# Kernel tuning notes

Hardware: AMD Instinct MI355X
Metric: run time of the kernel (lower is better)

The kernel has to match this reference:

```python
import jax, jax.numpy as jnp
import numpy as np

N = 100_000   # nodes
E = 1_600_000 # edges per edge type
DIN = 128     # input_dim
DH = 128      # prot_hidden_dim
L = 3         # prot_num_layers
EPS = 1e-5


def setup_inputs() -> dict:
    key = jax.random.key(0)
    ks = jax.random.split(key, 8)
    s = 1.0 / np.sqrt(DH)
    return {
        "x": jax.random.normal(ks[0], (N, DIN), jnp.float32),
        "src": jax.random.randint(ks[1], (3, E), 0, N, jnp.int32),
        "dst": jax.random.randint(ks[2], (3, E), 0, N, jnp.int32),
        "gc_W0": jax.random.normal(ks[3], (3, DIN, DH), jnp.float32) * s,
        "gc_b0": jnp.zeros((3, DH), jnp.float32),
        "gc_W": jax.random.normal(ks[4], (L - 1, 3, DH, DH), jnp.float32) * s,
        "gc_b": jnp.zeros((L - 1, 3, DH), jnp.float32),
        "fc_W": jax.random.normal(ks[5], (L, DH, DH), jnp.float32) * s,
        "fc_b": jnp.zeros((L, DH), jnp.float32),
        "bn_gamma": jnp.ones((L, DH), jnp.float32),
        "bn_beta": jnp.zeros((L, DH), jnp.float32),
    }


def _graph_conv(x, src, dst, W, b):
    # DGL GraphConv, norm='both': D_in^{-1/2} A D_out^{-1/2} X W + b
    ones = jnp.ones(src.shape[0], x.dtype)
    deg_out = jnp.clip(jax.ops.segment_sum(ones, src, num_segments=N), 1.0)
    deg_in = jnp.clip(jax.ops.segment_sum(ones, dst, num_segments=N), 1.0)
    # apply weight first (same math; keeps gathered message width = DH)
    h = (x * jax.lax.rsqrt(deg_out)[:, None]) @ W  # [N, DH]
    agg = jax.ops.segment_sum(h[src], dst, num_segments=N)  # gather + scatter-add
    return agg * jax.lax.rsqrt(deg_in)[:, None] + b


def _batchnorm(x, gamma, beta):
    # training-mode BatchNorm1d: biased batch statistics
    mu = jnp.mean(x, axis=0)
    var = jnp.mean(jnp.square(x - mu), axis=0)
    return (x - mu) * jax.lax.rsqrt(var + EPS) * gamma + beta


def reference(x, src, dst, gc_W0, gc_b0, gc_W, gc_b, fc_W, fc_b, bn_gamma, bn_beta):
    h = x
    for l in range(L):
        W = gc_W0 if l == 0 else gc_W[l - 1]
        b = gc_b0 if l == 0 else gc_b[l - 1]
        # HeteroGraphConv with aggregate='sum' over 3 edge types
        out = _graph_conv(h, src[0], dst[0], W[0], b[0])
        for e in range(1, 3):
            out = out + _graph_conv(h, src[e], dst[e], W[e], b[e])
        # FC -> ReLU -> BatchNorm (dropout = identity in eval mode)
        h = _batchnorm(jax.nn.relu(out @ fc_W[l] + fc_b[l]), bn_gamma[l], bn_beta[l])
    return h
```

## Files before the change

kernel.cpp:

```cpp
#include <hip/hip_runtime.h>


#define EPSV 1e-5f
#define CH 4096
#define MAXNB 512

typedef __attribute__((ext_vector_type(8))) short s8v;
typedef __attribute__((ext_vector_type(4))) float f4v;

__global__ void coarse_hist(const int* __restrict__ src, const int* __restrict__ dst,
                            int* __restrict__ chd, int* __restrict__ chs,
                            int E, int NB) {
    __shared__ int hd[MAXNB], hs[MAXNB];
    int t = blockIdx.y;
    for (int i = threadIdx.x; i < MAXNB; i += 256) { hd[i] = 0; hs[i] = 0; }
    __syncthreads();
    int base = blockIdx.x * CH;
    int end = base + CH < E ? base + CH : E;
    const int* sp = src + (size_t)t * E;
    const int* dp = dst + (size_t)t * E;
    for (int i = base + threadIdx.x; i < end; i += 256) {
        atomicAdd(&hd[dp[i] >> 8], 1);
        atomicAdd(&hs[sp[i] >> 8], 1);
    }
    __syncthreads();
    for (int b = threadIdx.x; b < NB; b += 256) {
        if (hd[b]) atomicAdd(&chd[t * NB + b], hd[b]);
        if (hs[b]) atomicAdd(&chs[t * NB + b], hs[b]);
    }
}

__global__ void scan_off(const int* __restrict__ chd, const int* __restrict__ chs,
                         int* __restrict__ offd, int* __restrict__ offs,
                         int* __restrict__ gcd, int* __restrict__ gcs,
                         int* __restrict__ rowptr, int NB, int N, int E) {
    __shared__ int s[MAXNB];
    int tid = threadIdx.x;
    for (int a = 0; a < 6; ++a) {
        const int* h = (a < 3) ? chd + a * NB : chs + (a - 3) * NB;
        int* off = (a < 3) ? offd + a * (NB + 1) : offs + (a - 3) * (NB + 1);
        int* gc = (a < 3) ? gcd + a * NB : gcs + (a - 3) * NB;
        s[tid] = (tid < NB) ? h[tid] : 0;
        __syncthreads();
        for (int o = 1; o < MAXNB; o <<= 1) {
            int v = (tid >= o) ? s[tid - o] : 0;
            __syncthreads();
            s[tid] += v;
            __syncthreads();
        }
        if (tid < NB) {
            off[tid + 1] = s[tid];
            if (tid == 0) off[0] = 0;
        }
        __syncthreads();
        if (tid < NB) gc[tid] = off[tid];
        __syncthreads();
    }
    if (tid < 3) rowptr[tid * (N + 1) + N] = E;
}

__launch_bounds__(256)
__global__ void scatter_coarse(const int* __restrict__ src, const int* __restrict__ dst,
                               int* __restrict__ gcd, int* __restrict__ gcs,
                               int* __restrict__ dbuf, unsigned char* __restrict__ sbuf,
                               int E, int NB) {
    __shared__ int hd[MAXNB], hs[MAXNB];
    __shared__ int lod[MAXNB], los[MAXNB];
    __shared__ int bd[MAXNB], bs[MAXNB];
    __shared__ int rbi[CH];
    __shared__ unsigned char rbs[CH];
    const int tid = threadIdx.x;
    const int t = blockIdx.y;
    const int base = blockIdx.x * CH;
    const int end = base + CH < E ? base + CH : E;
    const int cnt = end - base;
    const int* sp = src + (size_t)t * E;
    const int* dp = dst + (size_t)t * E;

    for (int i = tid; i < MAXNB; i += 256) { hd[i] = 0; hs[i] = 0; }
    __syncthreads();
    for (int i = base + tid; i < end; i += 256) {
        atomicAdd(&hd[dp[i] >> 8], 1);
        atomicAdd(&hs[sp[i] >> 8], 1);
    }
    __syncthreads();
    for (int b = tid; b < NB; b += 256) {
        bd[b] = hd[b] ? atomicAdd(&gcd[t * NB + b], hd[b]) : 0;
        bs[b] = hs[b] ? atomicAdd(&gcs[t * NB + b], hs[b]) : 0;
    }
    lod[tid] = hd[tid]; lod[tid + 256] = hd[tid + 256];
    los[tid] = hs[tid]; los[tid + 256] = hs[tid + 256];
    __syncthreads();
    for (int o = 1; o < MAXNB; o <<= 1) {
        int a0 = lod[tid], a1 = lod[tid + 256];
        int b0 = los[tid], b1 = los[tid + 256];
        int p0 = (tid >= o) ? lod[tid - o] : 0;
        int p1 = lod[tid + 256 - o];
        int q0 = (tid >= o) ? los[tid - o] : 0;
        int q1 = los[tid + 256 - o];
        __syncthreads();
        lod[tid] = a0 + p0; lod[tid + 256] = a1 + p1;
        los[tid] = b0 + q0; los[tid + 256] = b1 + q1;
        __syncthreads();
    }
    hd[tid] = lod[tid] - hd[tid]; hd[tid + 256] = lod[tid + 256] - hd[tid + 256];
    hs[tid] = los[tid] - hs[tid]; hs[tid + 256] = los[tid + 256] - hs[tid + 256];
    __syncthreads();
    for (int i = base + tid; i < end; i += 256) {
        int sv = sp[i], dv = dp[i];
        int lp = atomicAdd(&hd[dv >> 8], 1);
        rbi[lp] = (sv << 8) | (dv & 255);
        int ls = atomicAdd(&hs[sv >> 8], 1);
        rbs[ls] = (unsigned char)(sv & 255);
    }
    __syncthreads();
    for (int i = tid; i < cnt; i += 256) {
        int lo = 0, hi = NB - 1;
        while (lo < hi) { int mid = (lo + hi) >> 1; if (lod[mid] > i) hi = mid; else lo = mid + 1; }
        int excl = lo ? lod[lo - 1] : 0;
        dbuf[(size_t)t * E + bd[lo] + (i - excl)] = rbi[i];
    }
    for (int i = tid; i < cnt; i += 256) {
        int lo = 0, hi = NB - 1;
        while (lo < hi) { int mid = (lo + hi) >> 1; if (los[mid] > i) hi = mid; else lo = mid + 1; }
        int excl = lo ? los[lo - 1] : 0;
        sbuf[(size_t)t * E + bs[lo] + (i - excl)] = rbs[i];
    }
}

#define FDCAP 6656
__global__ void fine_dst(const int* __restrict__ dbuf, const int* __restrict__ offd,
                         int* __restrict__ esrc, int* __restrict__ rowptr,
                         float* __restrict__ dri, int E, int N, int NB) {
    __shared__ int h[256], sc[256], cur[256];
    __shared__ int rb[FDCAP];
    int b = blockIdx.x, t = blockIdx.y;
    int tid = threadIdx.x;
    h[tid] = 0;
    __syncthreads();
    int beg = offd[t * (NB + 1) + b], end = offd[t * (NB + 1) + b + 1];
    int cnt = end - beg;
    const int* dp = dbuf + (size_t)t * E;
    for (int i = beg + tid; i < end; i += 256) atomicAdd(&h[dp[i] & 255], 1);
    __syncthreads();
    sc[tid] = h[tid];
    __syncthreads();
    for (int o = 1; o < 256; o <<= 1) {
        int v = (tid >= o) ? sc[tid - o] : 0;
        __syncthreads();
        sc[tid] += v;
        __syncthreads();
    }
    int excl = sc[tid] - h[tid];
    cur[tid] = excl;
    int node = b * 256 + tid;
    if (node < N) {
        rowptr[t * (N + 1) + node] = beg + excl;
        int dg = h[tid] < 1 ? 1 : h[tid];
        dri[(size_t)t * N + node] = rsqrtf((float)dg);
    }
    __syncthreads();
    if (cnt <= FDCAP) {
        for (int i = beg + tid; i < end; i += 256) {
            int v = dp[i];
            int p = atomicAdd(&cur[v & 255], 1);
            rb[p] = v >> 8;
        }
        __syncthreads();
        for (int i = tid; i < cnt; i += 256) esrc[(size_t)t * E + beg + i] = rb[i];
    } else {
        for (int i = beg + tid; i < end; i += 256) {
            int v = dp[i];
            int p = beg + atomicAdd(&cur[v & 255], 1);
            esrc[(size_t)t * E + p] = v >> 8;
        }
    }
}

__global__ void fine_src(const unsigned char* __restrict__ sbuf, const int* __restrict__ offs,
                         float* __restrict__ dro, int E, int N, int NB) {
    __shared__ int h[256];
    int b = blockIdx.x, t = blockIdx.y;
    int tid = threadIdx.x;
    h[tid] = 0;
    __syncthreads();
    int beg = offs[t * (NB + 1) + b], end = offs[t * (NB + 1) + b + 1];
    const unsigned char* sp = sbuf + (size_t)t * E;
    for (int i = beg + tid; i < end; i += 256) atomicAdd(&h[sp[i]], 1);
    __syncthreads();
    int node = b * 256 + tid;
    if (node < N) {
        int dg = h[tid] < 1 ? 1 : h[tid];
        dro[(size_t)t * N + node] = rsqrtf((float)dg);
    }
}

__device__ __forceinline__ unsigned int bfr(float f) {
    unsigned int u = __float_as_uint(f);
    return (u + 0x7FFFu + ((u >> 16) & 1u)) >> 16;
}
__device__ __forceinline__ unsigned int pack2(float lo, float hi) {
    return bfr(lo) | (bfr(hi) << 16);
}
__device__ __forceinline__ float blo(unsigned int u) { return __uint_as_float(u << 16); }
__device__ __forceinline__ float bhi(unsigned int u) { return __uint_as_float(u & 0xFFFF0000u); }

__global__ void cvt_bf16(const float* __restrict__ h, unsigned short* __restrict__ h2,
                         int total8) {
    int i = blockIdx.x * 256 + threadIdx.x;
    if (i >= total8) return;
    const float4* hp = (const float4*)h + (size_t)i * 2;
    float4 v0 = hp[0], v1 = hp[1];
    uint4 o;
    o.x = pack2(v0.x, v0.y);
    o.y = pack2(v0.z, v0.w);
    o.z = pack2(v1.x, v1.y);
    o.w = pack2(v1.z, v1.w);
    ((uint4*)h2)[i] = o;
}

__global__ void pack_w(const float* __restrict__ gcW0, const float* __restrict__ gcW,
                       const float* __restrict__ fcW, unsigned short* __restrict__ Wg,
                       unsigned short* __restrict__ Wf) {
    int mat = blockIdx.x;
    const float* srcp;
    unsigned short* dstp;
    if (mat < 9) {
        int l = mat / 3, e = mat % 3;
        srcp = (l == 0) ? gcW0 + (size_t)e * 16384
                        : gcW + ((size_t)(l - 1) * 3 + e) * 16384;
        dstp = Wg + (size_t)mat * 16384;
    } else {
        srcp = fcW + (size_t)(mat - 9) * 16384;
        dstp = Wf + (size_t)(mat - 9) * 16384;
    }
    for (int p = threadIdx.x; p < 16384; p += 256) {
        int j = p & 7;
        int ln = (p >> 3) & 63;
        int nt = (p >> 9) & 7;
        int ks = p >> 12;
        int k = ks * 32 + (ln >> 4) * 8 + j;
        int n = nt * 16 + (ln & 15);
        dstp[p] = (unsigned short)bfr(srcp[k * 128 + n]);
    }
}

__launch_bounds__(256)
__global__ void agg_kernel(const unsigned short* __restrict__ h2, const int* __restrict__ rowptrB,
                           const int* __restrict__ esrcB, const float* __restrict__ droB,
                           const float* __restrict__ driB, unsigned short* __restrict__ zB,
                           int N, int E) {
    const int e = blockIdx.y;
    const int* rowptr = rowptrB + e * (N + 1);
    const int* esrc = esrcB + (size_t)e * E;
    const float* dro = droB + (size_t)e * N;
    const float* dri = driB + (size_t)e * N;
    unsigned short* z = zB + (size_t)e * N * 128;

    int idx = blockIdx.x * 256 + threadIdx.x;
    int node = idx >> 4;
    int lq = idx & 15;
    if (node >= N) return;
    int beg = rowptr[node], end = rowptr[node + 1];
    const uint4* hp = (const uint4*)h2 + lq;
    float a0 = 0.f, a1 = 0.f, a2 = 0.f, a3 = 0.f, a4 = 0.f, a5 = 0.f, a6 = 0.f, a7 = 0.f;
    int j = beg;
    for (; j + 8 <= end; j += 8) {
        int s[8];
#pragma unroll
        for (int q = 0; q < 8; ++q) s[q] = esrc[j + q];
        uint4 u[8];
#pragma unroll
        for (int q = 0; q < 8; ++q) u[q] = hp[(size_t)s[q] * 16];
        float w[8];
#pragma unroll
        for (int q = 0; q < 8; ++q) w[q] = dro[s[q]];
#pragma unroll
        for (int q = 0; q < 8; ++q) {
            a0 += w[q] * blo(u[q].x); a1 += w[q] * bhi(u[q].x);
            a2 += w[q] * blo(u[q].y); a3 += w[q] * bhi(u[q].y);
            a4 += w[q] * blo(u[q].z); a5 += w[q] * bhi(u[q].z);
            a6 += w[q] * blo(u[q].w); a7 += w[q] * bhi(u[q].w);
        }
    }
    for (; j + 4 <= end; j += 4) {
        int s[4];
#pragma unroll
        for (int q = 0; q < 4; ++q) s[q] = esrc[j + q];
        uint4 u[4];
#pragma unroll
        for (int q = 0; q < 4; ++q) u[q] = hp[(size_t)s[q] * 16];
        float w[4];
#pragma unroll
        for (int q = 0; q < 4; ++q) w[q] = dro[s[q]];
#pragma unroll
        for (int q = 0; q < 4; ++q) {
            a0 += w[q] * blo(u[q].x); a1 += w[q] * bhi(u[q].x);
            a2 += w[q] * blo(u[q].y); a3 += w[q] * bhi(u[q].y);
            a4 += w[q] * blo(u[q].z); a5 += w[q] * bhi(u[q].z);
            a6 += w[q] * blo(u[q].w); a7 += w[q] * bhi(u[q].w);
        }
    }
    for (; j < end; ++j) {
        int s0 = esrc[j];
        float w0 = dro[s0];
        uint4 u0 = hp[(size_t)s0 * 16];
        a0 += w0 * blo(u0.x); a1 += w0 * bhi(u0.x);
        a2 += w0 * blo(u0.y); a3 += w0 * bhi(u0.y);
        a4 += w0 * blo(u0.z); a5 += w0 * bhi(u0.z);
        a6 += w0 * blo(u0.w); a7 += w0 * bhi(u0.w);
    }
    float scl = dri[node];
    uint4 o;
    o.x = pack2(a0 * scl, a1 * scl);
    o.y = pack2(a2 * scl, a3 * scl);
    o.z = pack2(a4 * scl, a5 * scl);
    o.w = pack2(a6 * scl, a7 * scl);
    ((uint4*)z)[(size_t)node * 16 + lq] = o;
}

__launch_bounds__(256)
__global__ void mfma_gc(const unsigned short* __restrict__ zB,
                        const unsigned short* __restrict__ Wp,
                        const float* __restrict__ b3,
                        unsigned short* __restrict__ C, int M) {
    const int tid = threadIdx.x;
    const int l = tid & 63;
    const int wv = tid >> 6;
    const int wm = wv >> 1, wn = wv & 1;
    const int m0 = blockIdx.x * 128;
    const int lr = l & 15;
    const int lk = (l >> 4) * 8;
    f4v acc[4][4];
#pragma unroll
    for (int i = 0; i < 4; ++i)
#pragma unroll
        for (int j = 0; j < 4; ++j) acc[i][j] = (f4v){0.f, 0.f, 0.f, 0.f};

    int rowb[4];
#pragma unroll
    for (int mt = 0; mt < 4; ++mt) {
        int r = m0 + wm * 64 + mt * 16 + lr;
        rowb[mt] = (r < M) ? r : (M - 1);
    }
#pragma unroll
    for (int e = 0; e < 3; ++e) {
        const unsigned short* zp = zB + (size_t)e * M * 128;
        const unsigned short* wp = Wp + (size_t)e * 16384;
#pragma unroll
        for (int ks = 0; ks < 4; ++ks) {
            s8v a[4], b[4];
#pragma unroll
            for (int mt = 0; mt < 4; ++mt)
                a[mt] = *(const s8v*)(zp + (size_t)rowb[mt] * 128 + ks * 32 + lk);
#pragma unroll
            for (int nt = 0; nt < 4; ++nt)
                b[nt] = *(const s8v*)(wp + ks * 4096 + (wn * 4 + nt) * 512 + l * 8);
#pragma unroll
            for (int mt = 0; mt < 4; ++mt)
#pragma unroll
                for (int nt = 0; nt < 4; ++nt)
                    acc[mt][nt] = __builtin_amdgcn_mfma_f32_16x16x32_bf16(
                        a[mt], b[nt], acc[mt][nt], 0, 0, 0);
        }
    }
    float bs[4];
    int col[4];
#pragma unroll
    for (int nt = 0; nt < 4; ++nt) {
        col[nt] = wn * 64 + nt * 16 + lr;
        bs[nt] = b3[col[nt]] + b3[128 + col[nt]] + b3[256 + col[nt]];
    }
#pragma unroll
    for (int mt = 0; mt < 4; ++mt) {
#pragma unroll
        for (int r = 0; r < 4; ++r) {
            int row = m0 + wm * 64 + mt * 16 + (l >> 4) * 4 + r;
            if (row < M) {
                unsigned short* cp = C + (size_t)row * 128;
#pragma unroll
                for (int nt = 0; nt < 4; ++nt)
                    cp[col[nt]] = (unsigned short)bfr(acc[mt][nt][r] + bs[nt]);
            }
        }
    }
}

template <int MODE>
__launch_bounds__(256)
__global__ void mfma_fc(const unsigned short* __restrict__ A,
                        const unsigned short* __restrict__ Wp,
                        const float* __restrict__ bias,
                        unsigned short* __restrict__ outb, float* __restrict__ outf,
                        float* __restrict__ bnsum, int M) {
    __shared__ float red[256];
    const int tid = threadIdx.x;
    const int l = tid & 63;
    const int wv = tid >> 6;
    const int wm = wv >> 1, wn = wv & 1;
    const int m0 = blockIdx.x * 128;
    const int lr = l & 15;
    const int lk = (l >> 4) * 8;
    f4v acc[4][4];
#pragma unroll
    for (int i = 0; i < 4; ++i)
#pragma unroll
        for (int j = 0; j < 4; ++j) acc[i][j] = (f4v){0.f, 0.f, 0.f, 0.f};

    int rowb[4];
#pragma unroll
    for (int mt = 0; mt < 4; ++mt) {
        int r = m0 + wm * 64 + mt * 16 + lr;
        rowb[mt] = (r < M) ? r : (M - 1);
    }
#pragma unroll
    for (int ks = 0; ks < 4; ++ks) {
        s8v a[4], b[4];
#pragma unroll
        for (int mt = 0; mt < 4; ++mt)
            a[mt] = *(const s8v*)(A + (size_t)rowb[mt] * 128 + ks * 32 + lk);
#pragma unroll
        for (int nt = 0; nt < 4; ++nt)
            b[nt] = *(const s8v*)(Wp + ks * 4096 + (wn * 4 + nt) * 512 + l * 8);
#pragma unroll
        for (int mt = 0; mt < 4; ++mt)
#pragma unroll
            for (int nt = 0; nt < 4; ++nt)
                acc[mt][nt] = __builtin_amdgcn_mfma_f32_16x16x32_bf16(
                    a[mt], b[nt], acc[mt][nt], 0, 0, 0);
    }

    float bv[4], cs[4] = {}, cq[4] = {};
    int col[4];
#pragma unroll
    for (int nt = 0; nt < 4; ++nt) {
        col[nt] = wn * 64 + nt * 16 + lr;
        bv[nt] = bias[col[nt]];
    }
#pragma unroll
    for (int mt = 0; mt < 4; ++mt) {
#pragma unroll
        for (int r = 0; r < 4; ++r) {
            int row = m0 + wm * 64 + mt * 16 + (l >> 4) * 4 + r;
            if (row < M) {
#pragma unroll
                for (int nt = 0; nt < 4; ++nt) {
                    float v = acc[mt][nt][r] + bv[nt];
                    v = v > 0.f ? v : 0.f;
                    cs[nt] += v;
                    cq[nt] += v * v;
                    if (MODE == 0)
                        outb[(size_t)row * 128 + col[nt]] = (unsigned short)bfr(v);
                    else
                        outf[(size_t)row * 128 + col[nt]] = v;
                }
            }
        }
    }
    red[tid] = 0.f;
    __syncthreads();
#pragma unroll
    for (int nt = 0; nt < 4; ++nt) {
        atomicAdd(&red[col[nt]], cs[nt]);
        atomicAdd(&red[128 + col[nt]], cq[nt]);
    }
    __syncthreads();
    if (tid < 128) {
        atomicAdd(&bnsum[tid], red[tid]);
        atomicAdd(&bnsum[128 + tid], red[128 + tid]);
    }
}

__global__ void bn_affine_bf16(unsigned short* __restrict__ h2, const float* __restrict__ bnsum,
                               const float* __restrict__ gamma, const float* __restrict__ beta,
                               float invn, int total8) {
    __shared__ float lss[256];
    int tid = threadIdx.x;
    if (tid < 128) {
        float mean = bnsum[tid] * invn;
        float var = bnsum[128 + tid] * invn - mean * mean;
        float sc = gamma[tid] * rsqrtf(var + EPSV);
        lss[tid] = sc;
        lss[128 + tid] = beta[tid] - mean * sc;
    }
    __syncthreads();
    int i = blockIdx.x * 256 + tid;
    if (i >= total8) return;
    uint4 v = ((const uint4*)h2)[i];
    int cb = (i & 15) * 8;
    float4 a0 = *(const float4*)&lss[cb];
    float4 a1 = *(const float4*)&lss[cb + 4];
    float4 b0 = *(const float4*)&lss[128 + cb];
    float4 b1 = *(const float4*)&lss[128 + cb + 4];
    uint4 o;
    o.x = pack2(blo(v.x) * a0.x + b0.x, bhi(v.x) * a0.y + b0.y);
    o.y = pack2(blo(v.y) * a0.z + b0.z, bhi(v.y) * a0.w + b0.w);
    o.z = pack2(blo(v.z) * a1.x + b1.x, bhi(v.z) * a1.y + b1.y);
    o.w = pack2(blo(v.w) * a1.z + b1.z, bhi(v.w) * a1.w + b1.w);
    ((uint4*)h2)[i] = o;
}

__global__ void bn_apply(float* __restrict__ h, const float* __restrict__ bnsum,
                         const float* __restrict__ gamma, const float* __restrict__ beta,
                         float invn, int total4) {
    __shared__ float lss[256];
    int tid = threadIdx.x;
    if (tid < 128) {
        float mean = bnsum[tid] * invn;
        float var = bnsum[128 + tid] * invn - mean * mean;
        float sc = gamma[tid] * rsqrtf(var + EPSV);
        lss[tid] = sc;
        lss[128 + tid] = beta[tid] - mean * sc;
    }
    __syncthreads();
    int i = blockIdx.x * 256 + tid;
    if (i >= total4) return;
    int c4 = (i & 31) * 4;
    float4 sc = *(const float4*)&lss[c4];
    float4 sh = *(const float4*)&lss[128 + c4];
    float4 v = ((float4*)h)[i];
    v.x = v.x * sc.x + sh.x;
    v.y = v.y * sc.y + sh.y;
    v.z = v.z * sc.z + sh.z;
    v.w = v.w * sc.w + sh.w;
    ((float4*)h)[i] = v;
}

extern "C" void kernel_launch(void* const* d_in, const int* in_sizes, int n_in,
                              void* d_out, int out_size, void* d_ws, size_t ws_size,
                              hipStream_t stream) {
    const float* x    = (const float*)d_in[0];
    const int*   src  = (const int*)d_in[1];
    const int*   dst  = (const int*)d_in[2];
    const float* gcW0 = (const float*)d_in[3];
    const float* gcb0 = (const float*)d_in[4];
    const float* gcW  = (const float*)d_in[5];
    const float* gcb  = (const float*)d_in[6];
    const float* fcW  = (const float*)d_in[7];
    const float* fcb  = (const float*)d_in[8];
    const float* bng  = (const float*)d_in[9];
    const float* bnb  = (const float*)d_in[10];
    float* out = (float*)d_out;

    const int N = in_sizes[0] / 128;
    const int E = in_sizes[1] / 3;
    const int NB = (N + 255) / 256;

    char* w = (char*)d_ws;
    auto alloc = [&](size_t bytes) -> char* {
        char* p = w;
        w += (bytes + 255) & ~(size_t)255;
        return p;
    };
    unsigned short* zB    = (unsigned short*)alloc((size_t)3 * N * 128 * 2);
    unsigned short* gcout = (unsigned short*)alloc((size_t)N * 128 * 2);
    unsigned short* h2    = (unsigned short*)alloc((size_t)N * 128 * 2);
    unsigned short* Wg    = (unsigned short*)alloc((size_t)9 * 16384 * 2);
    unsigned short* Wf    = (unsigned short*)alloc((size_t)3 * 16384 * 2);
    int*   esrc   = (int*)alloc((size_t)3 * E * 4);
    int*   rowptr = (int*)alloc((size_t)3 * (N + 1) * 4);
    float* dro    = (float*)alloc((size_t)3 * N * 4);
    float* dri    = (float*)alloc((size_t)3 * N * 4);
    int*   chd    = (int*)alloc((size_t)3 * NB * 4);
    int*   chs    = (int*)alloc((size_t)3 * NB * 4);
    int*   offd   = (int*)alloc((size_t)3 * (NB + 1) * 4);
    int*   offs   = (int*)alloc((size_t)3 * (NB + 1) * 4);
    int*   gcd    = (int*)alloc((size_t)3 * NB * 4);
    int*   gcs    = (int*)alloc((size_t)3 * NB * 4);
    float* bnsum  = (float*)alloc(256 * 4);
    int* dbuf = (int*)zB;
    unsigned char* sbuf = (unsigned char*)gcout;

    hipMemsetAsync(chd, 0, (size_t)3 * NB * 4, stream);
    hipMemsetAsync(chs, 0, (size_t)3 * NB * 4, stream);
    dim3 cg2((E + CH - 1) / CH, 3);
    coarse_hist<<<cg2, 256, 0, stream>>>(src, dst, chd, chs, E, NB);
    scan_off<<<1, MAXNB, 0, stream>>>(chd, chs, offd, offs, gcd, gcs, rowptr, NB, N, E);
    scatter_coarse<<<cg2, 256, 0, stream>>>(src, dst, gcd, gcs, dbuf, sbuf, E, NB);
    dim3 fg(NB, 3);
    fine_dst<<<fg, 256, 0, stream>>>(dbuf, offd, esrc, rowptr, dri, E, N, NB);
    fine_src<<<fg, 256, 0, stream>>>(sbuf, offs, dro, E, N, NB);

    pack_w<<<12, 256, 0, stream>>>(gcW0, gcW, fcW, Wg, Wf);
    const int cvtGrid = (N * 16 + 255) / 256;
    cvt_bf16<<<cvtGrid, 256, 0, stream>>>(x, h2, N * 16);

    const int gemmGrid = (N + 127) / 128;
    const float invn = 1.0f / (float)N;
    dim3 aggG((N * 16 + 255) / 256, 3);

    for (int l = 0; l < 3; ++l) {
        const float* bl = (l == 0) ? gcb0 : gcb + (size_t)(l - 1) * 3 * 128;
        agg_kernel<<<aggG, 256, 0, stream>>>(h2, rowptr, esrc, dro, dri, zB, N, E);
        mfma_gc<<<gemmGrid, 256, 0, stream>>>(zB, Wg + (size_t)l * 3 * 16384, bl, gcout, N);
        hipMemsetAsync(bnsum, 0, 256 * 4, stream);
        if (l < 2)
            mfma_fc<0><<<gemmGrid, 256, 0, stream>>>(gcout, Wf + (size_t)l * 16384,
                                                     fcb + (size_t)l * 128, h2, nullptr,
                                                     bnsum, N);
        else
            mfma_fc<1><<<gemmGrid, 256, 0, stream>>>(gcout, Wf + (size_t)l * 16384,
                                                     fcb + (size_t)l * 128, nullptr, out,
                                                     bnsum, N);
        if (l < 2)
            bn_affine_bf16<<<cvtGrid, 256, 0, stream>>>(h2, bnsum, bng + (size_t)l * 128,
                                                        bnb + (size_t)l * 128, invn, N * 16);
        else
            bn_apply<<<(N * 32 + 255) / 256, 256, 0, stream>>>(out, bnsum,
                                                               bng + (size_t)l * 128,
                                                               bnb + (size_t)l * 128, invn,
                                                               N * 32);
    }
}
```

Before: 997.3 us.

## Pack source degree weights with edge indices and fold BatchNorm affine into aggregation

Edge lists now store (src, rsqrt(out-degree)) pairs so the aggregation no longer does a dependent random gather of source weights. The BatchNorm affine for intermediate layers is applied algebraically inside the next layer's aggregation using the sum of edge weights, removing a separate read-modify-write pass over the features. This doubles edge-list bytes and slightly changes bf16 rounding since un-normalized activations are stored.

```diff
diff --git a/kernel.cpp b/kernel.cpp
--- a/kernel.cpp
+++ b/kernel.cpp
@@ -128,10 +128,29 @@
     }
 }
 
+__global__ void fine_src(const unsigned char* __restrict__ sbuf, const int* __restrict__ offs,
+                         float* __restrict__ dro, int E, int N, int NB) {
+    __shared__ int h[256];
+    int b = blockIdx.x, t = blockIdx.y;
+    int tid = threadIdx.x;
+    h[tid] = 0;
+    __syncthreads();
+    int beg = offs[t * (NB + 1) + b], end = offs[t * (NB + 1) + b + 1];
+    const unsigned char* sp = sbuf + (size_t)t * E;
+    for (int i = beg + tid; i < end; i += 256) atomicAdd(&h[sp[i]], 1);
+    __syncthreads();
+    int node = b * 256 + tid;
+    if (node < N) {
+        int dg = h[tid] < 1 ? 1 : h[tid];
+        dro[(size_t)t * N + node] = rsqrtf((float)dg);
+    }
+}
+
 #define FDCAP 6656
 __global__ void fine_dst(const int* __restrict__ dbuf, const int* __restrict__ offd,
-                         int* __restrict__ esrc, int* __restrict__ rowptr,
-                         float* __restrict__ dri, int E, int N, int NB) {
+                         const float* __restrict__ dro, int2* __restrict__ esrcw,
+                         int* __restrict__ rowptr, float* __restrict__ dri,
+                         int E, int N, int NB) {
     __shared__ int h[256], sc[256], cur[256];
     __shared__ int rb[FDCAP];
     int b = blockIdx.x, t = blockIdx.y;
@@ -141,6 +160,7 @@
     int beg = offd[t * (NB + 1) + b], end = offd[t * (NB + 1) + b + 1];
     int cnt = end - beg;
     const int* dp = dbuf + (size_t)t * E;
+    const float* drt = dro + (size_t)t * N;
     for (int i = beg + tid; i < end; i += 256) atomicAdd(&h[dp[i] & 255], 1);
     __syncthreads();
     sc[tid] = h[tid];
@@ -167,31 +187,17 @@
             rb[p] = v >> 8;
         }
         __syncthreads();
-        for (int i = tid; i < cnt; i += 256) esrc[(size_t)t * E + beg + i] = rb[i];
+        for (int i = tid; i < cnt; i += 256) {
+            int sv = rb[i];
+            esrcw[(size_t)t * E + beg + i] = make_int2(sv, __float_as_int(drt[sv]));
+        }
     } else {
         for (int i = beg + tid; i < end; i += 256) {
             int v = dp[i];
+            int sv = v >> 8;
             int p = beg + atomicAdd(&cur[v & 255], 1);
-            esrc[(size_t)t * E + p] = v >> 8;
-        }
-    }
-}
-
-__global__ void fine_src(const unsigned char* __restrict__ sbuf, const int* __restrict__ offs,
-                         float* __restrict__ dro, int E, int N, int NB) {
-    __shared__ int h[256];
-    int b = blockIdx.x, t = blockIdx.y;
-    int tid = threadIdx.x;
-    h[tid] = 0;
-    __syncthreads();
-    int beg = offs[t * (NB + 1) + b], end = offs[t * (NB + 1) + b + 1];
-    const unsigned char* sp = sbuf + (size_t)t * E;
-    for (int i = beg + tid; i < end; i += 256) atomicAdd(&h[sp[i]], 1);
-    __syncthreads();
-    int node = b * 256 + tid;
-    if (node < N) {
-        int dg = h[tid] < 1 ? 1 : h[tid];
-        dro[(size_t)t * N + node] = rsqrtf((float)dg);
+            esrcw[(size_t)t * E + p] = make_int2(sv, __float_as_int(drt[sv]));
+        }
     }
 }
 
@@ -245,15 +251,28 @@
     }
 }
 
+template <int AFF>
 __launch_bounds__(256)
 __global__ void agg_kernel(const unsigned short* __restrict__ h2, const int* __restrict__ rowptrB,
-                           const int* __restrict__ esrcB, const float* __restrict__ droB,
-                           const float* __restrict__ driB, unsigned short* __restrict__ zB,
-                           int N, int E) {
+                           const int2* __restrict__ esrcwB, const float* __restrict__ driB,
+                           const float* __restrict__ bnsum, const float* __restrict__ gamma,
+                           const float* __restrict__ beta, float invn,
+                           unsigned short* __restrict__ zB, int N, int E) {
+    __shared__ float lss[256];
+    if (AFF) {
+        int tid = threadIdx.x;
+        if (tid < 128) {
+            float mean = bnsum[tid] * invn;
+            float var = bnsum[128 + tid] * invn - mean * mean;
+            float sc = gamma[tid] * rsqrtf(var + EPSV);
+            lss[tid] = sc;
+            lss[128 + tid] = beta[tid] - mean * sc;
+        }
+        __syncthreads();
+    }
     const int e = blockIdx.y;
     const int* rowptr = rowptrB + e * (N + 1);
-    const int* esrc = esrcB + (size_t)e * E;
-    const float* dro = droB + (size_t)e * N;
+    const int2* esrcw = esrcwB + (size_t)e * E;
     const float* dri = driB + (size_t)e * N;
     unsigned short* z = zB + (size_t)e * N * 128;
 
@@ -264,53 +283,65 @@
     int beg = rowptr[node], end = rowptr[node + 1];
     const uint4* hp = (const uint4*)h2 + lq;
     float a0 = 0.f, a1 = 0.f, a2 = 0.f, a3 = 0.f, a4 = 0.f, a5 = 0.f, a6 = 0.f, a7 = 0.f;
+    float wacc = 0.f;
     int j = beg;
     for (; j + 8 <= end; j += 8) {
-        int s[8];
-#pragma unroll
-        for (int q = 0; q < 8; ++q) s[q] = esrc[j + q];
+        int2 r[8];
+#pragma unroll
+        for (int q = 0; q < 8; ++q) r[q] = esrcw[j + q];
         uint4 u[8];
 #pragma unroll
-        for (int q = 0; q < 8; ++q) u[q] = hp[(size_t)s[q] * 16];
-        float w[8];
-#pragma unroll
-        for (int q = 0; q < 8; ++q) w[q] = dro[s[q]];
+        for (int q = 0; q < 8; ++q) u[q] = hp[(size_t)r[q].x * 16];
 #pragma unroll
         for (int q = 0; q < 8; ++q) {
-            a0 += w[q] * blo(u[q].x); a1 += w[q] * bhi(u[q].x);
-            a2 += w[q] * blo(u[q].y); a3 += w[q] * bhi(u[q].y);
-            a4 += w[q] * blo(u[q].z); a5 += w[q] * bhi(u[q].z);
-            a6 += w[q] * blo(u[q].w); a7 += w[q] * bhi(u[q].w);
+            float w = __int_as_float(r[q].y);
+            if (AFF) wacc += w;
+            a0 += w * blo(u[q].x); a1 += w * bhi(u[q].x);
+            a2 += w * blo(u[q].y); a3 += w * bhi(u[q].y);
+            a4 += w * blo(u[q].z); a5 += w * bhi(u[q].z);
+            a6 += w * blo(u[q].w); a7 += w * bhi(u[q].w);
         }
     }
     for (; j + 4 <= end; j += 4) {
-        int s[4];
-#pragma unroll
-        for (int q = 0; q < 4; ++q) s[q] = esrc[j + q];
+        int2 r[4];
+#pragma unroll
+        for (int q = 0; q < 4; ++q) r[q] = esrcw[j + q];
         uint4 u[4];
 #pragma unroll
-        for (int q = 0; q < 4; ++q) u[q] = hp[(size_t)s[q] * 16];
-        float w[4];
-#pragma unroll
-        for (int q = 0; q < 4; ++q) w[q] = dro[s[q]];
+        for (int q = 0; q < 4; ++q) u[q] = hp[(size_t)r[q].x * 16];
 #pragma unroll
         for (int q = 0; q < 4; ++q) {
-            a0 += w[q] * blo(u[q].x); a1 += w[q] * bhi(u[q].x);
-            a2 += w[q] * blo(u[q].y); a3 += w[q] * bhi(u[q].y);
-            a4 += w[q] * blo(u[q].z); a5 += w[q] * bhi(u[q].z);
-            a6 += w[q] * blo(u[q].w); a7 += w[q] * bhi(u[q].w);
+            float w = __int_as_float(r[q].y);
+            if (AFF) wacc += w;
+            a0 += w * blo(u[q].x); a1 += w * bhi(u[q].x);
+            a2 += w * blo(u[q].y); a3 += w * bhi(u[q].y);
+            a4 += w * blo(u[q].z); a5 += w * bhi(u[q].z);
+            a6 += w * blo(u[q].w); a7 += w * bhi(u[q].w);
         }
     }
     for (; j < end; ++j) {
-        int s0 = esrc[j];
-        float w0 = dro[s0];
-        uint4 u0 = hp[(size_t)s0 * 16];
-        a0 += w0 * blo(u0.x); a1 += w0 * bhi(u0.x);
-        a2 += w0 * blo(u0.y); a3 += w0 * bhi(u0.y);
-        a4 += w0 * blo(u0.z); a5 += w0 * bhi(u0.z);
-        a6 += w0 * blo(u0.w); a7 += w0 * bhi(u0.w);
+        int2 r0 = esrcw[j];
+        float w = __int_as_float(r0.y);
+        if (AFF) wacc += w;
+        uint4 u0 = hp[(size_t)r0.x * 16];
+        a0 += w * blo(u0.x); a1 += w * bhi(u0.x);
+        a2 += w * blo(u0.y); a3 += w * bhi(u0.y);
+        a4 += w * blo(u0.z); a5 += w * bhi(u0.z);
+        a6 += w * blo(u0.w); a7 += w * bhi(u0.w);
     }
     float scl = dri[node];
+    if (AFF) {
+        const float* ap = &lss[lq * 8];
+        const float* bp = &lss[128 + lq * 8];
+        a0 = ap[0] * a0 + bp[0] * wacc;
+        a1 = ap[1] * a1 + bp[1] * wacc;
+        a2 = ap[2] * a2 + bp[2] * wacc;
+        a3 = ap[3] * a3 + bp[3] * wacc;
+        a4 = ap[4] * a4 + bp[4] * wacc;
+        a5 = ap[5] * a5 + bp[5] * wacc;
+        a6 = ap[6] * a6 + bp[6] * wacc;
+        a7 = ap[7] * a7 + bp[7] * wacc;
+    }
     uint4 o;
     o.x = pack2(a0 * scl, a1 * scl);
     o.y = pack2(a2 * scl, a3 * scl);
@@ -471,35 +502,6 @@
     }
 }
 
-__global__ void bn_affine_bf16(unsigned short* __restrict__ h2, const float* __restrict__ bnsum,
-                               const float* __restrict__ gamma, const float* __restrict__ beta,
-                               float invn, int total8) {
-    __shared__ float lss[256];
-    int tid = threadIdx.x;
-    if (tid < 128) {
-        float mean = bnsum[tid] * invn;
-        float var = bnsum[128 + tid] * invn - mean * mean;
-        float sc = gamma[tid] * rsqrtf(var + EPSV);
-        lss[tid] = sc;
-        lss[128 + tid] = beta[tid] - mean * sc;
-    }
-    __syncthreads();
-    int i = blockIdx.x * 256 + tid;
-    if (i >= total8) return;
-    uint4 v = ((const uint4*)h2)[i];
-    int cb = (i & 15) * 8;
-    float4 a0 = *(const float4*)&lss[cb];
-    float4 a1 = *(const float4*)&lss[cb + 4];
-    float4 b0 = *(const float4*)&lss[128 + cb];
-    float4 b1 = *(const float4*)&lss[128 + cb + 4];
-    uint4 o;
-    o.x = pack2(blo(v.x) * a0.x + b0.x, bhi(v.x) * a0.y + b0.y);
-    o.y = pack2(blo(v.y) * a0.z + b0.z, bhi(v.y) * a0.w + b0.w);
-    o.z = pack2(blo(v.z) * a1.x + b1.x, bhi(v.z) * a1.y + b1.y);
-    o.w = pack2(blo(v.w) * a1.z + b1.z, bhi(v.w) * a1.w + b1.w);
-    ((uint4*)h2)[i] = o;
-}
-
 __global__ void bn_apply(float* __restrict__ h, const float* __restrict__ bnsum,
                          const float* __restrict__ gamma, const float* __restrict__ beta,
                          float invn, int total4) {
@@ -557,7 +559,7 @@
     unsigned short* h2    = (unsigned short*)alloc((size_t)N * 128 * 2);
     unsigned short* Wg    = (unsigned short*)alloc((size_t)9 * 16384 * 2);
     unsigned short* Wf    = (unsigned short*)alloc((size_t)3 * 16384 * 2);
-    int*   esrc   = (int*)alloc((size_t)3 * E * 4);
+    int2*  esrcw  = (int2*)alloc((size_t)3 * E * 8);
     int*   rowptr = (int*)alloc((size_t)3 * (N + 1) * 4);
     float* dro    = (float*)alloc((size_t)3 * N * 4);
     float* dri    = (float*)alloc((size_t)3 * N * 4);
@@ -578,8 +580,8 @@
     scan_off<<<1, MAXNB, 0, stream>>>(chd, chs, offd, offs, gcd, gcs, rowptr, NB, N, E);
     scatter_coarse<<<cg2, 256, 0, stream>>>(src, dst, gcd, gcs, dbuf, sbuf, E, NB);
     dim3 fg(NB, 3);
-    fine_dst<<<fg, 256, 0, stream>>>(dbuf, offd, esrc, rowptr, dri, E, N, NB);
     fine_src<<<fg, 256, 0, stream>>>(sbuf, offs, dro, E, N, NB);
+    fine_dst<<<fg, 256, 0, stream>>>(dbuf, offd, dro, esrcw, rowptr, dri, E, N, NB);
 
     pack_w<<<12, 256, 0, stream>>>(gcW0, gcW, fcW, Wg, Wf);
     const int cvtGrid = (N * 16 + 255) / 256;
@@ -591,7 +593,15 @@
 
     for (int l = 0; l < 3; ++l) {
         const float* bl = (l == 0) ? gcb0 : gcb + (size_t)(l - 1) * 3 * 128;
-        agg_kernel<<<aggG, 256, 0, stream>>>(h2, rowptr, esrc, dro, dri, zB, N, E);
+        if (l == 0)
+            agg_kernel<0><<<aggG, 256, 0, stream>>>(h2, rowptr, esrcw, dri,
+                                                    nullptr, nullptr, nullptr, invn,
+                                                    zB, N, E);
+        else
+            agg_kernel<1><<<aggG, 256, 0, stream>>>(h2, rowptr, esrcw, dri,
+                                                    bnsum, bng + (size_t)(l - 1) * 128,
+                                                    bnb + (size_t)(l - 1) * 128, invn,
+                                                    zB, N, E);
         mfma_gc<<<gemmGrid, 256, 0, stream>>>(zB, Wg + (size_t)l * 3 * 16384, bl, gcout, N);
         hipMemsetAsync(bnsum, 0, 256 * 4, stream);
         if (l < 2)
@@ -602,13 +612,7 @@
             mfma_fc<1><<<gemmGrid, 256, 0, stream>>>(gcout, Wf + (size_t)l * 16384,
                                                      fcb + (size_t)l * 128, nullptr, out,
                                                      bnsum, N);
-        if (l < 2)
-            bn_affine_bf16<<<cvtGrid, 256, 0, stream>>>(h2, bnsum, bng + (size_t)l * 128,
-                                                        bnb + (size_t)l * 128, invn, N * 16);
-        else
-            bn_apply<<<(N * 32 + 255) / 256, 256, 0, stream>>>(out, bnsum,
-                                                               bng + (size_t)l * 128,
-                                                               bnb + (size_t)l * 128, invn,
-                                                               N * 32);
-    }
-}
+    }
+    bn_apply<<<(N * 32 + 255) / 256, 256, 0, stream>>>(out, bnsum, bng + 2 * 128,
+                                                       bnb + 2 * 128, invn, N * 32);
+}
```

Result: no change. 991.6 us (-0.6%).
